# Optimization experiments

Hardware: AMD Instinct MI355X
Metric: run time of the kernel (lower is better)

## Reference

```python
import jax, jax.numpy as jnp
import numpy as np

N, E, HIN, H, FC, C, G = 50000, 1600000, 7, 128, 256, 2, 512

def _glorot(k, shape):
    fan = shape[0] + shape[1]
    return jax.random.uniform(k, shape, jnp.float32, -1.0, 1.0) * jnp.sqrt(6.0 / fan)

def setup_inputs() -> dict:
    key = jax.random.key(0)
    ks = jax.random.split(key, 40)
    inp = {}
    inp['x'] = jax.random.normal(ks[0], (N, HIN), jnp.float32)
    inp['edge_index'] = jax.random.randint(ks[1], (2, E), 0, N)
    inp['batch'] = jnp.sort(jax.random.randint(ks[2], (N,), 0, G))
    dims = [(HIN, H), (H, H), (H, H)]
    for i, (di, do) in enumerate(dims):
        kk = jax.random.split(ks[3 + i], 3)
        inp[f'Wl{i}'] = _glorot(kk[0], (di, do))
        inp[f'bl{i}'] = jnp.zeros((do,), jnp.float32)
        inp[f'Wr{i}'] = _glorot(kk[1], (di, do))
        inp[f'br{i}'] = jnp.zeros((do,), jnp.float32)
        inp[f'att{i}'] = _glorot(kk[2], (1, do))[0]  # GATv2 att vector [H]
        inp[f'bo{i}'] = jnp.zeros((do,), jnp.float32)
    inp['fc1_W'] = _glorot(ks[10], (H, FC))
    inp['fc1_b'] = jnp.zeros((FC,), jnp.float32)
    inp['fc2_W'] = _glorot(ks[11], (FC, C))
    inp['fc2_b'] = jnp.zeros((C,), jnp.float32)
    return inp

def reference(x, edge_index, batch,
              Wl0, bl0, Wr0, br0, att0, bo0,
              Wl1, bl1, Wr1, br1, att1, bo1,
              Wl2, bl2, Wr2, br2, att2, bo2,
              fc1_W, fc1_b, fc2_W, fc2_b):
    n = x.shape[0]
    loop = jnp.arange(n)
    src = jnp.concatenate([edge_index[0], loop])  # self-loops (PyG default)
    dst = jnp.concatenate([edge_index[1], loop])

    def conv(h, Wl, bl, Wr, br, att, bo):
        xl = h @ Wl + bl               # [N,H] source transform
        xr = h @ Wr + br               # [N,H] target transform
        m = jax.nn.leaky_relu(xl[src] + xr[dst], 0.2)  # [E+N,H]
        e = m @ att                    # [E+N] attention logits
        emax = jax.ops.segment_max(e, dst, num_segments=n)
        w = jnp.exp(e - emax[dst])
        denom = jax.ops.segment_sum(w, dst, num_segments=n)
        alpha = w / denom[dst]         # per-target softmax
        return jax.ops.segment_sum(alpha[:, None] * xl[src], dst, num_segments=n) + bo

    h = jax.nn.elu(conv(x, Wl0, bl0, Wr0, br0, att0, bo0))
    h = jax.nn.elu(conv(h, Wl1, bl1, Wr1, br1, att1, bo1))
    h = jax.nn.elu(conv(h, Wl2, bl2, Wr2, br2, att2, bo2))

    # global_mean_pool
    sums = jax.ops.segment_sum(h, batch, num_segments=G)
    cnt = jax.ops.segment_sum(jnp.ones((n,), h.dtype), batch, num_segments=G)
    g = sums / jnp.maximum(cnt, 1.0)[:, None]

    z = jax.nn.relu(g @ fc1_W + fc1_b)
    logits = z @ fc2_W + fc2_b
    return jax.nn.log_softmax(logits, axis=1)
```

## Files before the change

### kernel.cpp

```cpp
#include <hip/hip_runtime.h>
#include <hip/hip_fp16.h>
#include <math.h>

#define H 128
#define FCD 256
#define BUKSH 7
#define MAXBUK 512

typedef _Float16 half8 __attribute__((ext_vector_type(8)));
typedef float floatx4 __attribute__((ext_vector_type(4)));
typedef float fv2 __attribute__((ext_vector_type(2)));

__device__ __forceinline__ fv2 h2fv2(__half2 h){
  float2 t = __half22float2(h);
  fv2 r; r.x = t.x; r.y = t.y; return r;
}

template<int CTRL>
__device__ __forceinline__ float dppadd(float x){
  return x + __int_as_float(__builtin_amdgcn_update_dpp(
      0, __float_as_int(x), CTRL, 0xf, 0xf, true));
}
__device__ __forceinline__ float grp16_sum(float x){
  x = dppadd<0x128>(x);
  x = dppadd<0x124>(x);
  x = dppadd<0x122>(x);
  x = dppadd<0x121>(x);
  return x;
}

__global__ void k_scan512(const int* __restrict__ in, int nb,
                          int* __restrict__ out1, int* __restrict__ out2){
  int t = threadIdx.x, lane = t & 63, w = t >> 6;
  int v = (t<nb) ? in[t] : 0;
  int x = v;
  #pragma unroll
  for (int off=1; off<64; off<<=1){
    int y = __shfl_up(x, off);
    if (lane >= off) x += y;
  }
  __shared__ int ws[8];
  if (lane==63) ws[w] = x;
  __syncthreads();
  int wo = 0;
  #pragma unroll
  for (int i=0;i<8;i++) if (i<w) wo += ws[i];
  int excl = wo + x - v;
  if (t<nb){ out1[t] = excl; if (out2) out2[t] = excl; }
  if (t==511) out1[nb] = wo + x;
}

__global__ void k_bhist(const int* __restrict__ ei, int E, int Et, int nbuk,
                        int* __restrict__ bhist){
  __shared__ int lh[MAXBUK];
  int t = threadIdx.x;
  lh[t] = 0;
  __syncthreads();
  int j0 = blockIdx.x*8192;
  #pragma unroll
  for (int i=0;i<16;i++){
    int j = j0 + i*512 + t;
    if (j < Et){
      int dst = (j < E) ? ei[E+j] : (j - E);
      atomicAdd(&lh[dst>>BUKSH], 1);
    }
  }
  __syncthreads();
  if (t < nbuk && lh[t]) atomicAdd(&bhist[t], lh[t]);
}

__global__ void k_bscatter(const int* __restrict__ ei, int E, int Et, int nbuk,
                           int* __restrict__ bnext, unsigned* __restrict__ ebuf){
  __shared__ int lh[MAXBUK];
  __shared__ int lbase[MAXBUK];
  int t = threadIdx.x;
  lh[t] = 0;
  __syncthreads();
  int j0 = blockIdx.x*8192;
  unsigned pk[16]; int bk[16]; int rk[16];
  #pragma unroll
  for (int i=0;i<16;i++){
    int j = j0 + i*512 + t;
    if (j < Et){
      int src, dst;
      if (j < E){ src = ei[j]; dst = ei[E+j]; } else { src = dst = j - E; }
      pk[i] = (unsigned)src | ((unsigned)dst << 16);
      bk[i] = dst >> BUKSH;
      rk[i] = atomicAdd(&lh[bk[i]], 1);
    }
  }
  __syncthreads();
  if (t < nbuk){
    int c = lh[t];
    lbase[t] = c ? atomicAdd(&bnext[t], c) : 0;
  }
  __syncthreads();
  #pragma unroll
  for (int i=0;i<16;i++){
    int j = j0 + i*512 + t;
    if (j < Et) ebuf[lbase[bk[i]] + rk[i]] = pk[i];
  }
}

__global__ void k_bfill(const unsigned* __restrict__ ebuf, const int* __restrict__ bbase,
                        int N, int Et,
                        int* __restrict__ row_ptr, int* __restrict__ deg,
                        int* __restrict__ csr, int* __restrict__ histsT){
  __shared__ int cnt[1<<BUKSH];
  __shared__ int lnxt[1<<BUKSH];
  __shared__ int bh[256];
  __shared__ int ws0[1];
  int b = blockIdx.x, t = threadIdx.x;
  if (t < (1<<BUKSH)) cnt[t] = 0;
  bh[t] = 0;
  if (b==0 && t==0) row_ptr[N] = Et;
  __syncthreads();
  int lo = bbase[b], hi = bbase[b+1];
  for (int j = lo + t; j < hi; j += 256){
    unsigned d = ebuf[j] >> 16;
    atomicAdd(&cnt[d & ((1<<BUKSH)-1)], 1);
  }
  __syncthreads();
  int lane = t & 63;
  int v = (t < (1<<BUKSH)) ? cnt[t] : 0;
  int x = v;
  #pragma unroll
  for (int off=1; off<64; off<<=1){
    int y = __shfl_up(x, off);
    if (lane >= off) x += y;
  }
  if (t==63) ws0[0] = x;
  __syncthreads();
  if (t >= 64 && t < 128) x += ws0[0];
  if (t < (1<<BUKSH)){
    int node = (b<<BUKSH) + t;
    int excl = lo + x - v;
    lnxt[t] = excl;
    if (node < N){
      row_ptr[node] = excl;
      deg[node] = v;
      atomicAdd(&bh[min(v,255)], 1);
    }
  }
  __syncthreads();
  histsT[t*MAXBUK + b] = bh[t];
  for (int j = lo + t; j < hi; j += 256){
    unsigned e = ebuf[j];
    int d = (e >> 16) & ((1<<BUKSH)-1);
    int r = atomicAdd(&lnxt[d], 1);
    csr[r] = (int)((e & 0xffff) << 8);
  }
}

__global__ void k_dbinscan(int* __restrict__ histsT, int nb, int* __restrict__ bintot){
  int d = blockIdx.x;
  int t = threadIdx.x, lane = t & 63, w = t >> 6;
  int v = (t<nb) ? histsT[d*MAXBUK + t] : 0;
  int x = v;
  #pragma unroll
  for (int off=1; off<64; off<<=1){
    int y = __shfl_up(x, off);
    if (lane >= off) x += y;
  }
  __shared__ int ws[8];
  if (lane==63) ws[w] = x;
  __syncthreads();
  int wo = 0;
  #pragma unroll
  for (int i=0;i<8;i++) if (i<w) wo += ws[i];
  if (t<nb) histsT[d*MAXBUK + t] = wo + x - v;
  if (t==511) bintot[d] = wo + x;
}

__global__ void k_dscatter2(const int* __restrict__ deg, int N,
                            const int* __restrict__ histsT, const int* __restrict__ bintot,
                            int* __restrict__ perm){
  __shared__ int lh[256];
  __shared__ int sbase[256];
  __shared__ int ws[4];
  int t = threadIdx.x, b = blockIdx.x;
  int lane = t & 63, w = t >> 6;
  int v = bintot[t];
  int x = v;
  #pragma unroll
  for (int off=1; off<64; off<<=1){
    int y = __shfl_up(x, off);
    if (lane >= off) x += y;
  }
  if (lane==63) ws[w] = x;
  lh[t] = 0;
  __syncthreads();
  int wo = (w>0?ws[0]:0) + (w>1?ws[1]:0) + (w>2?ws[2]:0);
  sbase[t] = wo + x - v;
  __syncthreads();
  if (t < 128){
    int i = (b<<BUKSH) + t;
    if (i < N){
      int d = min(deg[i],255);
      int r = atomicAdd(&lh[d], 1);
      perm[sbase[d] + histsT[d*MAXBUK + b] + r] = i;
    }
  }
}

__global__ void k_prep(const float* __restrict__ Wl1, const float* __restrict__ Wr1,
                       const float* __restrict__ Wl2, const float* __restrict__ Wr2,
                       _Float16* __restrict__ Wt, int* __restrict__ bhist){
  int idx = blockIdx.x*256 + threadIdx.x;
  if (blockIdx.x == 0){
    for (int i = threadIdx.x; i <= MAXBUK; i += 256) bhist[i] = 0;
  }
  int e    = idx & 7;
  int lane = (idx >> 3) & 63;
  int kb   = (idx >> 9) & 3;
  int nt   = (idx >> 11) & 15;
  int L    = idx >> 15;
  int m16 = lane & 15, quad = lane >> 4;
  int k = kb*32 + quad*8 + e;
  int n = nt*16 + m16;
  const float* W = (L==0) ? (n<H?Wl1:Wr1) : (n<H?Wl2:Wr2);
  Wt[idx] = (_Float16)W[k*H + (n&127)];
}

__global__ void k_gemm7(const float* __restrict__ x,
                        const float* __restrict__ Wl, const float* __restrict__ bl,
                        const float* __restrict__ Wr, const float* __restrict__ br,
                        __half* __restrict__ xl, __half* __restrict__ xr, int n){
  int col = threadIdx.x;
  int n0 = blockIdx.x*8;
  float accl[8], accr[8];
  float bL = bl[col], bR = br[col];
  #pragma unroll
  for (int t=0;t<8;t++){ accl[t]=bL; accr[t]=bR; }
  #pragma unroll
  for (int k=0;k<7;k++){
    float wl = Wl[k*H + col];
    float wr = Wr[k*H + col];
    #pragma unroll
    for (int t=0;t<8;t++){
      int node = n0+t; if (node >= n) node = n-1;
      float hv = x[(size_t)node*7 + k];
      accl[t] = fmaf(hv, wl, accl[t]);
      accr[t] = fmaf(hv, wr, accr[t]);
    }
  }
  #pragma unroll
  for (int t=0;t<8;t++){
    int node = n0+t;
    if (node < n){
      xl[(size_t)node*H + col] = __float2half(accl[t]);
      xr[(size_t)node*H + col] = __float2half(accr[t]);
    }
  }
}

__global__ __launch_bounds__(256) void k_gemm2h(
    const __half* __restrict__ h, const _Float16* __restrict__ Wt,
    const float* __restrict__ bl, const float* __restrict__ br,
    __half* __restrict__ xl, __half* __restrict__ xr, int n){
  int wave = threadIdx.x >> 6, lane = threadIdx.x & 63;
  int m16 = lane & 15, quad = lane >> 4;
  int row0 = blockIdx.x*64 + wave*16;
  int arow = row0 + m16; if (arow >= n) arow = n-1;
  const __half* hr = h + (size_t)arow*H;
  half8 a[4];
  #pragma unroll
  for (int kb=0;kb<4;kb++) a[kb] = *(const half8*)(hr + kb*32 + quad*8);
  floatx4 acc[16];
  #pragma unroll
  for (int t=0;t<16;t++){ floatx4 z = {0.f,0.f,0.f,0.f}; acc[t] = z; }
  #pragma unroll
  for (int nt=0;nt<16;nt++){
    const _Float16* bp = Wt + ((size_t)nt*4)*512 + lane*8;
    #pragma unroll
    for (int kb=0;kb<4;kb++){
      half8 b = *(const half8*)(bp + kb*512);
      acc[nt] = __builtin_amdgcn_mfma_f32_16x16x32_f16(a[kb], b, acc[nt], 0,0,0);
    }
  }
  #pragma unroll
  for (int nt=0;nt<16;nt++){
    int c = nt*16 + m16;
    float bias; __half* dst; int cc;
    if (c < H){ bias = bl[c];   dst = xl; cc = c;   }
    else      { bias = br[c-H]; dst = xr; cc = c-H; }
    #pragma unroll
    for (int r=0;r<4;r++){
      int rw = row0 + quad*4 + r;
      if (rw < n) dst[(size_t)rw*H + cc] = __float2half(acc[nt][r] + bias);
    }
  }
}

__global__ void k_gat(const __half* __restrict__ xl, const __half* __restrict__ xr,
                      const float* __restrict__ att, const float* __restrict__ bo,
                      const int* __restrict__ row_ptr, const int* __restrict__ csr_src,
                      const int* __restrict__ perm,
                      __half* __restrict__ hout, int n){
  int gid0 = (int)((blockIdx.x*blockDim.x + threadIdx.x) >> 4);
  int lane16 = threadIdx.x & 15;
  if (gid0 >= n) return;
  int gid = perm[n-1-gid0];
  const char* xlb = (const char*)xl + lane16*16;
  int f = lane16*8;
  fv2 xr2[4], a6[4], a4[4];
  {
    union { float4 q; __half2 h[4]; } U;
    U.q = *(const float4*)(xr + (size_t)gid*H + f);
    #pragma unroll
    for (int i=0;i<4;i++) xr2[i] = h2fv2(U.h[i]);
    float4 q0 = *(const float4*)(att + f);
    float4 q1 = *(const float4*)(att + f + 4);
    fv2 av[4];
    av[0].x=q0.x; av[0].y=q0.y; av[1].x=q0.z; av[1].y=q0.w;
    av[2].x=q1.x; av[2].y=q1.y; av[3].x=q1.z; av[3].y=q1.w;
    #pragma unroll
    for (int i=0;i<4;i++){ a6[i] = av[i]*0.6f; a4[i] = av[i]*0.4f; }
  }
  fv2 acc2[4];
  #pragma unroll
  for (int i=0;i<4;i++){ acc2[i].x = 0.f; acc2[i].y = 0.f; }
  float mmax = -INFINITY, denom = 0.f;
  int beg = row_ptr[gid], end = row_ptr[gid+1];
  int j = beg;
  for (; j+7 < end; j += 8){
    int s[8];
    #pragma unroll
    for (int u=0;u<8;u++) s[u] = csr_src[j+u];
    float4 r[8];
    #pragma unroll
    for (int u=0;u<8;u++) r[u] = *(const float4*)(xlb + s[u]);
    float d[8];
    #pragma unroll
    for (int u=0;u<8;u++){
      union { float4 q; __half2 h[4]; } U; U.q = r[u];
      fv2 d2; d2.x = 0.f; d2.y = 0.f;
      #pragma unroll
      for (int i=0;i<4;i++){
        fv2 uu = h2fv2(U.h[i]) + xr2[i];
        d2 += uu * a6[i];
        d2 += __builtin_elementwise_abs(uu) * a4[i];
      }
      d[u] = d2.x + d2.y;
    }
    #pragma unroll
    for (int u=0;u<8;u++) d[u] = grp16_sum(d[u]);
    float m8 = fmaxf(fmaxf(fmaxf(d[0],d[1]), fmaxf(d[2],d[3])),
                     fmaxf(fmaxf(d[4],d[5]), fmaxf(d[6],d[7])));
    if (m8 > mmax){
      float sc = __expf(mmax - m8);
      #pragma unroll
      for (int i=0;i<4;i++) acc2[i] *= sc;
      denom *= sc;
      mmax = m8;
    }
    #pragma unroll
    for (int u=0;u<8;u++){
      float w = __expf(d[u] - mmax);
      denom += w;
      union { float4 q; __half2 h[4]; } U; U.q = r[u];
      #pragma unroll
      for (int i=0;i<4;i++) acc2[i] += h2fv2(U.h[i]) * w;
    }
  }
  for (; j<end; j++){
    int s0 = csr_src[j];
    union { float4 q; __half2 h[4]; } U;
    U.q = *(const float4*)(xlb + s0);
    fv2 v2[4];
    #pragma unroll
    for (int i=0;i<4;i++) v2[i] = h2fv2(U.h[i]);
    fv2 d2; d2.x = 0.f; d2.y = 0.f;
    #pragma unroll
    for (int i=0;i<4;i++){
      fv2 uu = v2[i] + xr2[i];
      d2 += uu * a6[i];
      d2 += __builtin_elementwise_abs(uu) * a4[i];
    }
    float dd = d2.x + d2.y;
    dd = grp16_sum(dd);
    if (dd > mmax){
      float sc = __expf(mmax - dd);
      #pragma unroll
      for (int i=0;i<4;i++) acc2[i] *= sc;
      denom *= sc;
      mmax = dd;
    }
    float w = __expf(dd - mmax);
    denom += w;
    #pragma unroll
    for (int i=0;i<4;i++) acc2[i] += v2[i] * w;
  }
  float inv = 1.f/denom;
  float o[8];
  {
    float4 b0 = *(const float4*)(bo + f);
    float4 b1 = *(const float4*)(bo + f + 4);
    float bb[8] = {b0.x,b0.y,b0.z,b0.w,b1.x,b1.y,b1.z,b1.w};
    #pragma unroll
    for (int i=0;i<4;i++){
      float t0 = acc2[i].x*inv + bb[2*i];
      float t1 = acc2[i].y*inv + bb[2*i+1];
      o[2*i]   = t0 > 0.f ? t0 : expm1f(t0);
      o[2*i+1] = t1 > 0.f ? t1 : expm1f(t1);
    }
  }
  union { float4 f4; __half2 h2[4]; } u;
  #pragma unroll
  for (int i=0;i<4;i++) u.h2[i] = __floats2half2_rn(o[2*i], o[2*i+1]);
  *(float4*)(hout + (size_t)gid*H + f) = u.f4;
}

__global__ void k_fc(const __half* __restrict__ hbuf, const int* __restrict__ batch, int N,
                     const float* __restrict__ W1, const float* __restrict__ b1,
                     const float* __restrict__ W2, const float* __restrict__ b2,
                     float* __restrict__ out){
  __shared__ float g[H];
  __shared__ float2 part[4][64];
  __shared__ float zs[FCD];
  __shared__ int bounds[2];
  int gi = blockIdx.x;
  int t = threadIdx.x;
  if (t < 2){
    int target = gi + t;
    int lo = 0, hi = N;
    while (lo < hi){ int mid = (lo+hi)>>1; if (batch[mid] < target) lo = mid+1; else hi = mid; }
    bounds[t] = lo;
  }
  __syncthreads();
  int lo = bounds[0], hi = bounds[1];
  int pairc = t & 63, slice = t >> 6;
  float sx = 0.f, sy = 0.f;
  for (int node = lo + slice; node < hi; node += 4){
    float2 f2 = __half22float2(*(const __half2*)(hbuf + (size_t)node*H + pairc*2));
    sx += f2.x; sy += f2.y;
  }
  part[slice][pairc] = make_float2(sx, sy);
  __syncthreads();
  if (t < 64){
    float2 a = part[0][t], b = part[1][t], c = part[2][t], d = part[3][t];
    float cnt = (float)(hi - lo); if (cnt < 1.f) cnt = 1.f;
    float inv = 1.f/cnt;
    g[2*t]   = (a.x+b.x+c.x+d.x)*inv;
    g[2*t+1] = (a.y+b.y+c.y+d.y)*inv;
  }
  __syncthreads();
  float acc = b1[t];
  for (int k=0;k<H;k++) acc = fmaf(g[k], W1[k*FCD+t], acc);
  zs[t] = acc > 0.f ? acc : 0.f;
  __syncthreads();
  if (t < 2){
    float l = b2[t];
    for (int k=0;k<FCD;k++) l = fmaf(zs[k], W2[k*2+t], l);
    g[t] = l;
  }
  __syncthreads();
  if (t < 2){
    float l0 = g[0], l1 = g[1];
    float mx = fmaxf(l0,l1);
    float lse = mx + logf(__expf(l0-mx) + __expf(l1-mx));
    out[gi*2+t] = g[t] - lse;
  }
}

extern "C" void kernel_launch(void* const* d_in, const int* in_sizes, int n_in,
                              void* d_out, int out_size, void* d_ws, size_t ws_size,
                              hipStream_t stream) {
  const float* x     = (const float*)d_in[0];
  const int*   ei    = (const int*)  d_in[1];
  const int*   batch = (const int*)  d_in[2];
  const float* Wl[3]  = {(const float*)d_in[3],  (const float*)d_in[9],  (const float*)d_in[15]};
  const float* bl[3]  = {(const float*)d_in[4],  (const float*)d_in[10], (const float*)d_in[16]};
  const float* Wr[3]  = {(const float*)d_in[5],  (const float*)d_in[11], (const float*)d_in[17]};
  const float* br[3]  = {(const float*)d_in[6],  (const float*)d_in[12], (const float*)d_in[18]};
  const float* att[3] = {(const float*)d_in[7],  (const float*)d_in[13], (const float*)d_in[19]};
  const float* bo[3]  = {(const float*)d_in[8],  (const float*)d_in[14], (const float*)d_in[20]};
  const float* fc1W = (const float*)d_in[21];
  const float* fc1b = (const float*)d_in[22];
  const float* fc2W = (const float*)d_in[23];
  const float* fc2b = (const float*)d_in[24];

  const int N  = in_sizes[2];
  const int E  = in_sizes[1]/2;
  const int Et = E + N;
  const int G  = out_size/2;
  const int NBUK = (N + (1<<BUKSH)-1) >> BUKSH;
  const int NEB = (Et + 8191)/8192;

  char* p = (char*)d_ws;
  auto alloc = [&](size_t bytes)->void*{
    void* r = (void*)p; p += (bytes + 255) & ~(size_t)255; return r;
  };
  int*      deg     = (int*)     alloc((size_t)N*4);
  int*      row_ptr = (int*)     alloc((size_t)(N+1)*4);
  int*      bhist   = (int*)     alloc((size_t)(MAXBUK+1)*4);
  int*      bbase   = (int*)     alloc((size_t)(MAXBUK+1)*4);
  int*      bnext   = (int*)     alloc((size_t)(MAXBUK+1)*4);
  int*      histsT  = (int*)     alloc((size_t)256*MAXBUK*4);
  int*      bintot  = (int*)     alloc((size_t)260*4);
  int*      perm    = (int*)     alloc((size_t)N*4);
  int*      csr     = (int*)     alloc((size_t)Et*4);
  unsigned* ebuf    = (unsigned*)alloc((size_t)Et*4);
  __half*   xl      = (__half*)  alloc((size_t)N*H*2);
  __half*   xr      = (__half*)  alloc((size_t)N*H*2);
  __half*   hbuf    = (__half*)  alloc((size_t)N*H*2);
  _Float16* Wt      = (_Float16*)alloc((size_t)2*16*4*512*2);

  k_prep<<<256, 256, 0, stream>>>(Wl[1], Wr[1], Wl[2], Wr[2], Wt, bhist);

  k_bhist   <<<NEB, 512, 0, stream>>>(ei, E, Et, NBUK, bhist);
  k_scan512 <<<1, 512, 0, stream>>>(bhist, NBUK, bbase, bnext);
  k_bscatter<<<NEB, 512, 0, stream>>>(ei, E, Et, NBUK, bnext, ebuf);
  k_bfill   <<<NBUK, 256, 0, stream>>>(ebuf, bbase, N, Et, row_ptr, deg, csr, histsT);
  k_dbinscan<<<256, 512, 0, stream>>>(histsT, NBUK, bintot);
  k_dscatter2<<<NBUK, 256, 0, stream>>>(deg, N, histsT, bintot, perm);

  const int g7  = (N + 7)/8;
  const int gM  = (N + 63)/64;
  const int gg  = (int)(((size_t)N*16 + 255)/256);

  k_gemm7<<<g7, 128, 0, stream>>>(x, Wl[0], bl[0], Wr[0], br[0], xl, xr, N);
  k_gat<<<gg, 256, 0, stream>>>(xl, xr, att[0], bo[0], row_ptr, csr, perm, hbuf, N);
  k_gemm2h<<<gM, 256, 0, stream>>>(hbuf, Wt, bl[1], br[1], xl, xr, N);
  k_gat<<<gg, 256, 0, stream>>>(xl, xr, att[1], bo[1], row_ptr, csr, perm, hbuf, N);
  k_gemm2h<<<gM, 256, 0, stream>>>(hbuf, Wt + (size_t)16*4*512, bl[2], br[2], xl, xr, N);
  k_gat<<<gg, 256, 0, stream>>>(xl, xr, att[2], bo[2], row_ptr, csr, perm, hbuf, N);

  k_fc<<<G, 256, 0, stream>>>(hbuf, batch, N, fc1W, fc1b, fc2W, fc2b, (float*)d_out);
}
```

Before: 407.6 us.

## Fuse setup kernels and replace global degree sort with per-bucket sort

Merges the layer-0 projection, weight repacking and bucket histogram into one multi-role kernel. Per-block histograms are written to rows and reduced in the scan instead of using global atomics. The degree-ordered permutation is now computed locally within each 128-node bucket inside the CSR fill kernel, which removes two kernels and the global degree scan. The trade-off is weaker global degree ordering for the attention kernels' load balance.

Result: slower. 459.0 us (+12.6%).

```diff
diff --git a/kernel.cpp b/kernel.cpp
--- a/kernel.cpp
+++ b/kernel.cpp
@@ -29,10 +29,81 @@
   return x;
 }
 
-__global__ void k_scan512(const int* __restrict__ in, int nb,
-                          int* __restrict__ out1, int* __restrict__ out2){
+__global__ __launch_bounds__(256) void k_setup(
+    const float* __restrict__ x,
+    const float* __restrict__ Wl0, const float* __restrict__ bl0,
+    const float* __restrict__ Wr0, const float* __restrict__ br0,
+    __half* __restrict__ xl, __half* __restrict__ xr, int n,
+    const float* __restrict__ Wl1, const float* __restrict__ Wr1,
+    const float* __restrict__ Wl2, const float* __restrict__ Wr2,
+    _Float16* __restrict__ Wt,
+    const int* __restrict__ ei, int E, int Et, int* __restrict__ bhistM,
+    int NB7, int NEB){
+  __shared__ int lh[MAXBUK];
+  int b = blockIdx.x, t = threadIdx.x;
+  if (b < NB7){
+    int col = t & 127;
+    int n0 = b*16 + (t >> 7)*8;
+    float accl[8], accr[8];
+    float bL = bl0[col], bR = br0[col];
+    #pragma unroll
+    for (int q=0;q<8;q++){ accl[q]=bL; accr[q]=bR; }
+    #pragma unroll
+    for (int k=0;k<7;k++){
+      float wl = Wl0[k*H + col];
+      float wr = Wr0[k*H + col];
+      #pragma unroll
+      for (int q=0;q<8;q++){
+        int node = n0+q; if (node >= n) node = n-1;
+        float hv = x[(size_t)node*7 + k];
+        accl[q] = fmaf(hv, wl, accl[q]);
+        accr[q] = fmaf(hv, wr, accr[q]);
+      }
+    }
+    #pragma unroll
+    for (int q=0;q<8;q++){
+      int node = n0+q;
+      if (node < n){
+        xl[(size_t)node*H + col] = __float2half(accl[q]);
+        xr[(size_t)node*H + col] = __float2half(accr[q]);
+      }
+    }
+  } else if (b < NB7 + 256){
+    int idx = (b - NB7)*256 + t;
+    int e    = idx & 7;
+    int lane = (idx >> 3) & 63;
+    int kb   = (idx >> 9) & 3;
+    int nt   = (idx >> 11) & 15;
+    int L    = idx >> 15;
+    int m16 = lane & 15, quad = lane >> 4;
+    int k = kb*32 + quad*8 + e;
+    int nn = nt*16 + m16;
+    const float* W = (L==0) ? (nn<H?Wl1:Wr1) : (nn<H?Wl2:Wr2);
+    Wt[idx] = (_Float16)W[k*H + (nn&127)];
+  } else {
+    int r = b - NB7 - 256;
+    lh[t] = 0; lh[t+256] = 0;
+    __syncthreads();
+    int j0 = r*8192;
+    #pragma unroll 4
+    for (int i=0;i<32;i++){
+      int j = j0 + i*256 + t;
+      if (j < Et){
+        int dst = (j < E) ? ei[E+j] : (j - E);
+        atomicAdd(&lh[dst>>BUKSH], 1);
+      }
+    }
+    __syncthreads();
+    bhistM[r*MAXBUK + t]       = lh[t];
+    bhistM[r*MAXBUK + 256 + t] = lh[t+256];
+  }
+}
+
+__global__ void k_scanB(const int* __restrict__ bhistM, int nrows,
+                        int* __restrict__ bbase, int* __restrict__ bnext){
   int t = threadIdx.x, lane = t & 63, w = t >> 6;
-  int v = (t<nb) ? in[t] : 0;
+  int v = 0;
+  for (int r=0; r<nrows; r++) v += bhistM[r*MAXBUK + t];
   int x = v;
   #pragma unroll
   for (int off=1; off<64; off<<=1){
@@ -46,27 +117,8 @@
   #pragma unroll
   for (int i=0;i<8;i++) if (i<w) wo += ws[i];
   int excl = wo + x - v;
-  if (t<nb){ out1[t] = excl; if (out2) out2[t] = excl; }
-  if (t==511) out1[nb] = wo + x;
-}
-
-__global__ void k_bhist(const int* __restrict__ ei, int E, int Et, int nbuk,
-                        int* __restrict__ bhist){
-  __shared__ int lh[MAXBUK];
-  int t = threadIdx.x;
-  lh[t] = 0;
-  __syncthreads();
-  int j0 = blockIdx.x*8192;
-  #pragma unroll
-  for (int i=0;i<16;i++){
-    int j = j0 + i*512 + t;
-    if (j < Et){
-      int dst = (j < E) ? ei[E+j] : (j - E);
-      atomicAdd(&lh[dst>>BUKSH], 1);
-    }
-  }
-  __syncthreads();
-  if (t < nbuk && lh[t]) atomicAdd(&bhist[t], lh[t]);
+  bbase[t] = excl; bnext[t] = excl;
+  if (t==511) bbase[512] = wo + x;
 }
 
 __global__ void k_bscatter(const int* __restrict__ ei, int E, int Et, int nbuk,
@@ -104,15 +156,18 @@
 
 __global__ void k_bfill(const unsigned* __restrict__ ebuf, const int* __restrict__ bbase,
                         int N, int Et,
-                        int* __restrict__ row_ptr, int* __restrict__ deg,
-                        int* __restrict__ csr, int* __restrict__ histsT){
+                        int* __restrict__ row_ptr, int* __restrict__ csr,
+                        int* __restrict__ perm){
   __shared__ int cnt[1<<BUKSH];
   __shared__ int lnxt[1<<BUKSH];
   __shared__ int bh[256];
+  __shared__ int sbase[256];
+  __shared__ int rk[256];
   __shared__ int ws0[1];
+  __shared__ int ws2[4];
   int b = blockIdx.x, t = threadIdx.x;
   if (t < (1<<BUKSH)) cnt[t] = 0;
-  bh[t] = 0;
+  bh[t] = 0; rk[t] = 0;
   if (b==0 && t==0) row_ptr[N] = Et;
   __syncthreads();
   int lo = bbase[b], hi = bbase[b+1];
@@ -122,8 +177,8 @@
   }
   __syncthreads();
   int lane = t & 63;
-  int v = (t < (1<<BUKSH)) ? cnt[t] : 0;
-  int x = v;
+  int mydeg = (t < (1<<BUKSH)) ? cnt[t] : 0;
+  int x = mydeg;
   #pragma unroll
   for (int off=1; off<64; off<<=1){
     int y = __shfl_up(x, off);
@@ -132,125 +187,39 @@
   if (t==63) ws0[0] = x;
   __syncthreads();
   if (t >= 64 && t < 128) x += ws0[0];
+  int node = (b<<BUKSH) + t;
   if (t < (1<<BUKSH)){
-    int node = (b<<BUKSH) + t;
-    int excl = lo + x - v;
+    int excl = lo + x - mydeg;
     lnxt[t] = excl;
     if (node < N){
       row_ptr[node] = excl;
-      deg[node] = v;
-      atomicAdd(&bh[min(v,255)], 1);
-    }
-  }
-  __syncthreads();
-  histsT[t*MAXBUK + b] = bh[t];
+      atomicAdd(&bh[min(mydeg,255)], 1);
+    }
+  }
+  __syncthreads();
   for (int j = lo + t; j < hi; j += 256){
     unsigned e = ebuf[j];
     int d = (e >> 16) & ((1<<BUKSH)-1);
     int r = atomicAdd(&lnxt[d], 1);
     csr[r] = (int)((e & 0xffff) << 8);
   }
-}
-
-__global__ void k_dbinscan(int* __restrict__ histsT, int nb, int* __restrict__ bintot){
-  int d = blockIdx.x;
-  int t = threadIdx.x, lane = t & 63, w = t >> 6;
-  int v = (t<nb) ? histsT[d*MAXBUK + t] : 0;
-  int x = v;
+  int bv = bh[t];
+  int bx = bv;
+  int w2 = t >> 6;
   #pragma unroll
   for (int off=1; off<64; off<<=1){
-    int y = __shfl_up(x, off);
-    if (lane >= off) x += y;
-  }
-  __shared__ int ws[8];
-  if (lane==63) ws[w] = x;
-  __syncthreads();
-  int wo = 0;
-  #pragma unroll
-  for (int i=0;i<8;i++) if (i<w) wo += ws[i];
-  if (t<nb) histsT[d*MAXBUK + t] = wo + x - v;
-  if (t==511) bintot[d] = wo + x;
-}
-
-__global__ void k_dscatter2(const int* __restrict__ deg, int N,
-                            const int* __restrict__ histsT, const int* __restrict__ bintot,
-                            int* __restrict__ perm){
-  __shared__ int lh[256];
-  __shared__ int sbase[256];
-  __shared__ int ws[4];
-  int t = threadIdx.x, b = blockIdx.x;
-  int lane = t & 63, w = t >> 6;
-  int v = bintot[t];
-  int x = v;
-  #pragma unroll
-  for (int off=1; off<64; off<<=1){
-    int y = __shfl_up(x, off);
-    if (lane >= off) x += y;
-  }
-  if (lane==63) ws[w] = x;
-  lh[t] = 0;
-  __syncthreads();
-  int wo = (w>0?ws[0]:0) + (w>1?ws[1]:0) + (w>2?ws[2]:0);
-  sbase[t] = wo + x - v;
-  __syncthreads();
-  if (t < 128){
-    int i = (b<<BUKSH) + t;
-    if (i < N){
-      int d = min(deg[i],255);
-      int r = atomicAdd(&lh[d], 1);
-      perm[sbase[d] + histsT[d*MAXBUK + b] + r] = i;
-    }
-  }
-}
-
-__global__ void k_prep(const float* __restrict__ Wl1, const float* __restrict__ Wr1,
-                       const float* __restrict__ Wl2, const float* __restrict__ Wr2,
-                       _Float16* __restrict__ Wt, int* __restrict__ bhist){
-  int idx = blockIdx.x*256 + threadIdx.x;
-  if (blockIdx.x == 0){
-    for (int i = threadIdx.x; i <= MAXBUK; i += 256) bhist[i] = 0;
-  }
-  int e    = idx & 7;
-  int lane = (idx >> 3) & 63;
-  int kb   = (idx >> 9) & 3;
-  int nt   = (idx >> 11) & 15;
-  int L    = idx >> 15;
-  int m16 = lane & 15, quad = lane >> 4;
-  int k = kb*32 + quad*8 + e;
-  int n = nt*16 + m16;
-  const float* W = (L==0) ? (n<H?Wl1:Wr1) : (n<H?Wl2:Wr2);
-  Wt[idx] = (_Float16)W[k*H + (n&127)];
-}
-
-__global__ void k_gemm7(const float* __restrict__ x,
-                        const float* __restrict__ Wl, const float* __restrict__ bl,
-                        const float* __restrict__ Wr, const float* __restrict__ br,
-                        __half* __restrict__ xl, __half* __restrict__ xr, int n){
-  int col = threadIdx.x;
-  int n0 = blockIdx.x*8;
-  float accl[8], accr[8];
-  float bL = bl[col], bR = br[col];
-  #pragma unroll
-  for (int t=0;t<8;t++){ accl[t]=bL; accr[t]=bR; }
-  #pragma unroll
-  for (int k=0;k<7;k++){
-    float wl = Wl[k*H + col];
-    float wr = Wr[k*H + col];
-    #pragma unroll
-    for (int t=0;t<8;t++){
-      int node = n0+t; if (node >= n) node = n-1;
-      float hv = x[(size_t)node*7 + k];
-      accl[t] = fmaf(hv, wl, accl[t]);
-      accr[t] = fmaf(hv, wr, accr[t]);
-    }
-  }
-  #pragma unroll
-  for (int t=0;t<8;t++){
-    int node = n0+t;
-    if (node < n){
-      xl[(size_t)node*H + col] = __float2half(accl[t]);
-      xr[(size_t)node*H + col] = __float2half(accr[t]);
-    }
+    int y = __shfl_up(bx, off);
+    if (lane >= off) bx += y;
+  }
+  if (lane==63) ws2[w2] = bx;
+  __syncthreads();
+  int wo = (w2>0?ws2[0]:0) + (w2>1?ws2[1]:0) + (w2>2?ws2[2]:0);
+  sbase[t] = wo + bx - bv;
+  __syncthreads();
+  if (t < (1<<BUKSH) && node < N){
+    int d = min(mydeg,255);
+    int r = atomicAdd(&rk[d], 1);
+    perm[(b<<BUKSH) + sbase[d] + r] = node;
   }
 }
 
@@ -486,18 +455,16 @@
   const int G  = out_size/2;
   const int NBUK = (N + (1<<BUKSH)-1) >> BUKSH;
   const int NEB = (Et + 8191)/8192;
+  const int NB7 = (N + 15)/16;
 
   char* p = (char*)d_ws;
   auto alloc = [&](size_t bytes)->void*{
     void* r = (void*)p; p += (bytes + 255) & ~(size_t)255; return r;
   };
-  int*      deg     = (int*)     alloc((size_t)N*4);
   int*      row_ptr = (int*)     alloc((size_t)(N+1)*4);
-  int*      bhist   = (int*)     alloc((size_t)(MAXBUK+1)*4);
-  int*      bbase   = (int*)     alloc((size_t)(MAXBUK+1)*4);
-  int*      bnext   = (int*)     alloc((size_t)(MAXBUK+1)*4);
-  int*      histsT  = (int*)     alloc((size_t)256*MAXBUK*4);
-  int*      bintot  = (int*)     alloc((size_t)260*4);
+  int*      bbase   = (int*)     alloc((size_t)(MAXBUK+8)*4);
+  int*      bnext   = (int*)     alloc((size_t)(MAXBUK+8)*4);
+  int*      bhistM  = (int*)     alloc((size_t)NEB*MAXBUK*4);
   int*      perm    = (int*)     alloc((size_t)N*4);
   int*      csr     = (int*)     alloc((size_t)Et*4);
   unsigned* ebuf    = (unsigned*)alloc((size_t)Et*4);
@@ -506,20 +473,17 @@
   __half*   hbuf    = (__half*)  alloc((size_t)N*H*2);
   _Float16* Wt      = (_Float16*)alloc((size_t)2*16*4*512*2);
 
-  k_prep<<<256, 256, 0, stream>>>(Wl[1], Wr[1], Wl[2], Wr[2], Wt, bhist);
-
-  k_bhist   <<<NEB, 512, 0, stream>>>(ei, E, Et, NBUK, bhist);
-  k_scan512 <<<1, 512, 0, stream>>>(bhist, NBUK, bbase, bnext);
+  k_setup<<<NB7 + 256 + NEB, 256, 0, stream>>>(
+      x, Wl[0], bl[0], Wr[0], br[0], xl, xr, N,
+      Wl[1], Wr[1], Wl[2], Wr[2], Wt,
+      ei, E, Et, bhistM, NB7, NEB);
+  k_scanB<<<1, 512, 0, stream>>>(bhistM, NEB, bbase, bnext);
   k_bscatter<<<NEB, 512, 0, stream>>>(ei, E, Et, NBUK, bnext, ebuf);
-  k_bfill   <<<NBUK, 256, 0, stream>>>(ebuf, bbase, N, Et, row_ptr, deg, csr, histsT);
-  k_dbinscan<<<256, 512, 0, stream>>>(histsT, NBUK, bintot);
-  k_dscatter2<<<NBUK, 256, 0, stream>>>(deg, N, histsT, bintot, perm);
-
-  const int g7  = (N + 7)/8;
+  k_bfill<<<NBUK, 256, 0, stream>>>(ebuf, bbase, N, Et, row_ptr, csr, perm);
+
   const int gM  = (N + 63)/64;
   const int gg  = (int)(((size_t)N*16 + 255)/256);
 
-  k_gemm7<<<g7, 128, 0, stream>>>(x, Wl[0], bl[0], Wr[0], br[0], xl, xr, N);
   k_gat<<<gg, 256, 0, stream>>>(xl, xr, att[0], bo[0], row_ptr, csr, perm, hbuf, N);
   k_gemm2h<<<gM, 256, 0, stream>>>(hbuf, Wt, bl[1], br[1], xl, xr, N);
   k_gat<<<gg, 256, 0, stream>>>(xl, xr, att[1], bo[1], row_ptr, csr, perm, hbuf, N);
```
